# Performance work log

Hardware: AMD Instinct MI355X
Metric: run time of the kernel (lower is better)

## Reference

```python
import jax, jax.numpy as jnp
import numpy as np

V, E, H, L, F, NQ, C = 32000, 256, 8, 4, 1024, 256, 10
B, S = 8, 1024
DK = E // H


def setup_inputs() -> dict:
    key = jax.random.key(0)
    ks = jax.random.split(key, 10)
    f = lambda k, shape, s=0.02: jax.random.normal(k, shape, jnp.float32) * s
    return {
        'tokens': jax.random.randint(ks[0], (B, S), 0, V, jnp.int32),
        'emb': f(ks[1], (V, E), 1.0),
        'theta_attn': f(ks[2], (L, H, DK), 0.5),
        'Wc': f(ks[3], (L, E, E)),
        'bc': jnp.zeros((L, E), jnp.float32),
        'g1': jnp.ones((L, E), jnp.float32),
        'bn1': jnp.zeros((L, E), jnp.float32),
        'theta_ffn': f(ks[4], (L, NQ), 0.5),
        'W1': f(ks[5], (L, NQ, F)),
        'b1': jnp.zeros((L, F), jnp.float32),
        'W2': f(ks[6], (L, F, E)),
        'b2': jnp.zeros((L, E), jnp.float32),
        'g2': jnp.ones((L, E), jnp.float32),
        'bn2': jnp.zeros((L, E), jnp.float32),
        'Wcls': f(ks[7], (E, C)),
        'bcls': jnp.zeros((C,), jnp.float32),
    }


def _ln(x, g, b, eps=1e-5):
    m = x.mean(-1, keepdims=True)
    v = ((x - m) ** 2).mean(-1, keepdims=True)
    return (x - m) / jnp.sqrt(v + eps) * g + b


def _pos_encoding(seq, dim):
    pos = jnp.arange(seq, dtype=jnp.float32)[:, None]
    div = jnp.exp(jnp.arange(0, dim, 2, dtype=jnp.float32) * (-np.log(10000.0) / dim))
    pe = jnp.zeros((seq, dim), jnp.float32)
    pe = pe.at[:, 0::2].set(jnp.sin(pos * div)).at[:, 1::2].set(jnp.cos(pos * div))
    return pe


def _qattn_proj(xh, theta):
    # xh: [B,S,H,dk], theta: [H,dk]. Circuit RX(x+th) per wire, CNOT ring, <Z_i>.
    # Analytic: <Z_i> = prod_{j<=i} cos(phi_j) for i>=1; <Z_0> = prod_{j>=1} cos(phi_j)
    c = jnp.cos(xh + theta)              # [B,S,H,dk]
    cum = jnp.cumprod(c, axis=-1)        # cum[...,i] = prod_{j<=i} c_j
    head0 = jnp.prod(c[..., 1:], axis=-1, keepdims=True)
    return jnp.concatenate([head0, cum[..., 1:]], axis=-1)  # [B,S,H,dk]


def _forward(tokens, emb, theta_attn, Wc, bc, g1, bn1, theta_ffn, W1, b1, W2, b2, g2, bn2, Wcls, bcls):
    b, s = tokens.shape
    x = emb[tokens] + _pos_encoding(s, E)  # [B,S,E]
    scale = 1.0 / np.sqrt(DK)
    for l in range(L):
        # quantum multi-head projection; q = k = v (same deterministic circuit)
        xh = x.reshape(b, s, H, DK)
        p = _qattn_proj(xh, theta_attn[l]).reshape(b, s, E)
        scores = jax.nn.softmax(jnp.einsum('bqe,bke->bqk', p, p) * scale, axis=-1)
        attn = jnp.einsum('bqk,bke->bqe', scores, p) @ Wc[l] + bc[l]
        x = _ln(x + attn, g1[l], bn1[l])
        # quantum FFN: <Z_i> = cos(x_i) * cos(theta_i), NQ == E here
        q = jnp.cos(x[..., :NQ]) * jnp.cos(theta_ffn[l])
        f = jax.nn.relu(q @ W1[l] + b1[l]) @ W2[l] + b2[l]
        x = _ln(x + f, g2[l], bn2[l])
    return x.mean(axis=1) @ Wcls + bcls  # [B,C]


def reference(tokens, emb, theta_attn, Wc, bc, g1, bn1, theta_ffn, W1, b1, W2, b2, g2, bn2, Wcls, bcls):
    return _forward(tokens, emb, theta_attn, Wc, bc, g1, bn1, theta_ffn, W1, b1, W2, b2, g2, bn2, Wcls, bcls)
```

## Files before the change

kernel.cpp:

```cpp
#include <hip/hip_runtime.h>
#include <hip/hip_bf16.h>
#include <math.h>

#define BB 8
#define SS 1024
#define EE 256
#define HH 8
#define DKK 32
#define LL 4
#define FF 1024
#define NQQ 256
#define CC 10

typedef __attribute__((ext_vector_type(8))) short short8;
typedef __attribute__((ext_vector_type(4))) short s16x4;
typedef __attribute__((ext_vector_type(4))) float f32x4;

static __device__ __forceinline__ f32x4 mfma16(short8 a, short8 b, f32x4 c) {
    return __builtin_amdgcn_mfma_f32_16x16x32_bf16(a, b, c, 0, 0, 0);
}
static __device__ __forceinline__ short f2bf(float f) {
    __hip_bfloat16 h = __float2bfloat16(f);
    return *reinterpret_cast<short*>(&h);
}

#define FRAG(P, tile, KG, kg, l) ((P) + (((size_t)((tile)*(KG) + (kg)))*64 + (l))*8)

static __device__ __forceinline__ void qproj_row(
        const float* __restrict__ xrow,
        const float* __restrict__ th,
        int b, int s, int h,
        short* __restrict__ PQ, short* __restrict__ PT) {
    float v[DKK];
    float cum = __cosf(xrow[h * DKK + 0] + th[0]);
    float prod1 = 1.0f;
    #pragma unroll
    for (int j = 1; j < DKK; ++j) {
        float c = __cosf(xrow[h * DKK + j] + th[j]);
        cum *= c;
        prod1 *= c;
        v[j] = cum;
    }
    v[0] = prod1;
    short* pq = PQ + (size_t)b * SS * EE;
    int stile = s >> 4, lr = s & 15;
    #pragma unroll
    for (int lg = 0; lg < 4; ++lg) {
        short8 u;
        #pragma unroll
        for (int j = 0; j < 8; ++j) u[j] = f2bf(v[lg*8 + j]);
        *(short8*)FRAG(pq, stile*8 + h, 1, 0, lg*16 + lr) = u;
    }
    short* pt = PT + (size_t)b * SS * EE;
    int kt = s >> 5, lgs = (s >> 3) & 3, j0 = s & 7;
    #pragma unroll
    for (int j = 0; j < DKK; ++j) {
        int e = h * DKK + j;
        FRAG(pt, e >> 4, 32, kt, lgs*16 + (e & 15))[j0] = f2bf(v[j]);
    }
}

__global__ __launch_bounds__(256) void k_prep(
        const float* __restrict__ W1, const float* __restrict__ W2,
        const float* __restrict__ Wc,
        short* __restrict__ W1P, short* __restrict__ W2P, short* __restrict__ WcP,
        const int* __restrict__ tokens, const float* __restrict__ emb,
        const float* __restrict__ theta_q,
        float* __restrict__ x, short* __restrict__ PQ, short* __restrict__ PT) {
    __shared__ float shmem[16 * 268];
    const int t = threadIdx.x;
    if (blockIdx.x < 2304) {
        int bid = blockIdx.x;
        int lyr = bid / 576, rem = bid % 576;
        const float* in; short* out; int R, C, tile;
        if (rem < 256)      { in = W1 + (size_t)lyr*NQQ*FF; out = W1P + (size_t)lyr*FF*NQQ; R = NQQ; C = FF;  tile = rem; }
        else if (rem < 512) { in = W2 + (size_t)lyr*FF*EE;  out = W2P + (size_t)lyr*EE*FF;  R = FF;  C = EE;  tile = rem - 256; }
        else                { in = Wc + (size_t)lyr*EE*EE;  out = WcP + (size_t)lyr*EE*EE;  R = EE;  C = EE;  tile = rem - 512; }
        const int KG = R >> 5;
        int tiles_c = C >> 5;
        int tc = tile % tiles_c, tr = tile / tiles_c;
        float (*tl)[33] = (float(*)[33])shmem;
        int rr = t >> 5, cc = t & 31;
        #pragma unroll
        for (int i = 0; i < 4; ++i)
            tl[rr + i*8][cc] = in[(size_t)(tr*32 + rr + i*8) * C + tc*32 + cc];
        __syncthreads();
        int ro = t >> 3, co = (t & 7) * 4;
        int n = tc*32 + ro;
        int k = tr*32 + co;
        int ntile = n >> 4, lr = n & 15;
        int kg = k >> 5, lg = (k & 31) >> 3, j0 = k & 7;
        s16x4 v;
        v[0] = f2bf(tl[co + 0][ro]);
        v[1] = f2bf(tl[co + 1][ro]);
        v[2] = f2bf(tl[co + 2][ro]);
        v[3] = f2bf(tl[co + 3][ro]);
        *(s16x4*)(FRAG(out, ntile, KG, kg, lg*16 + lr) + j0) = v;
    } else {
        int blk = blockIdx.x - 2304;
        int bsw = blk & 7, local = blk >> 3;
        int tok0 = bsw * SS + local * 16;
        {
            int r = t >> 4, c0 = (t & 15) * 16;
            int bs = tok0 + r;
            int s  = bs & (SS - 1);
            int tok = tokens[bs];
            const float* er = emb + (size_t)tok * EE + c0;
            float vals[16];
            #pragma unroll
            for (int i = 0; i < 16; ++i) {
                int col = c0 + i;
                int i2 = col >> 1;
                float div = __expf(-(float)(2 * i2) * (logf(10000.0f) / (float)EE));
                float ang = (float)s * div;
                float pe = (col & 1) ? __cosf(ang) : __sinf(ang);
                vals[i] = er[i] + pe;
                shmem[r * 268 + col] = vals[i];
            }
            float* xg = x + (size_t)bs * EE + c0;
            #pragma unroll
            for (int i4 = 0; i4 < 4; ++i4)
                *(float4*)(xg + i4 * 4) = *(const float4*)&vals[i4 * 4];
        }
        __syncthreads();
        if (t < 128) {
            int sl = t >> 3, h = t & 7;
            int bs = tok0 + sl;
            qproj_row(&shmem[sl * 268], theta_q + h * DKK,
                      bs >> 10, bs & (SS - 1), h, PQ, PT);
        }
    }
}

__global__ __launch_bounds__(256) void k_attn7(const short* __restrict__ PQ,
                                               const short* __restrict__ PT,
                                               short* __restrict__ YP) {
    const int b   = blockIdx.x & 7;
    const int qt  = blockIdx.x >> 3;
    const int tid = threadIdx.x;
    const int w   = tid >> 6;
    const int l   = tid & 63;
    const int lr  = l & 15, lg = l >> 4;
    const short* pq = PQ + (size_t)b * SS * EE;
    const short* pt = PT + (size_t)b * SS * EE;

    __shared__ float accP[2][16][264];
    __shared__ float lsL[4][16];
    __shared__ short wlds[4][16 * 40];

    short8 qf[8];
    #pragma unroll
    for (int kg = 0; kg < 8; ++kg)
        qf[kg] = *(const short8*)FRAG(pq, qt*8 + kg, 1, 0, l);

    f32x4 acc[16];
    #pragma unroll
    for (int i = 0; i < 16; ++i) acc[i] = f32x4{0.f, 0.f, 0.f, 0.f};
    float ls[4] = {0.f, 0.f, 0.f, 0.f};
    const float scale = 0.17677669529663687f;
    short* wl = wlds[w];

    for (int i = 0; i < 8; ++i) {
        const int kt = w + 4 * i;
        short8 sb0[8], sb1[8];
        #pragma unroll
        for (int kg = 0; kg < 8; ++kg) {
            sb0[kg] = *(const short8*)FRAG(pq, (2*kt)*8   + kg, 1, 0, l);
            sb1[kg] = *(const short8*)FRAG(pq, (2*kt+1)*8 + kg, 1, 0, l);
        }
        f32x4 s0a = {0.f,0.f,0.f,0.f}, s0b = {0.f,0.f,0.f,0.f};
        f32x4 s1a = {0.f,0.f,0.f,0.f}, s1b = {0.f,0.f,0.f,0.f};
        __builtin_amdgcn_s_setprio(1);
        #pragma unroll
        for (int kg = 0; kg < 4; ++kg) {
            s0a = mfma16(qf[kg], sb0[kg], s0a);
            s1a = mfma16(qf[kg], sb1[kg], s1a);
        }
        #pragma unroll
        for (int kg = 4; kg < 8; ++kg) {
            s0b = mfma16(qf[kg], sb0[kg], s0b);
            s1b = mfma16(qf[kg], sb1[kg], s1b);
        }
        __builtin_amdgcn_s_setprio(0);
        short8 pvb0[8];
        #pragma unroll
        for (int nt = 0; nt < 8; ++nt)
            pvb0[nt] = *(const short8*)FRAG(pt, nt, 32, kt, l);

        #pragma unroll
        for (int r = 0; r < 4; ++r) {
            float p0 = __expf((s0a[r] + s0b[r]) * scale);
            float p1 = __expf((s1a[r] + s1b[r]) * scale);
            ls[r] += p0 + p1;
            int q = lg * 4 + r;
            wl[q * 40 + lr]      = f2bf(p0);
            wl[q * 40 + 16 + lr] = f2bf(p1);
        }
        short8 pa = *(const short8*)(wl + lr * 40 + lg * 8);
        short8 pvb1[8];
        #pragma unroll
        for (int nt = 0; nt < 8; ++nt)
            pvb1[nt] = *(const short8*)FRAG(pt, 8 + nt, 32, kt, l);
        __builtin_amdgcn_s_setprio(1);
        #pragma unroll
        for (int nt = 0; nt < 8; ++nt)
            acc[nt] = mfma16(pa, pvb0[nt], acc[nt]);
        #pragma unroll
        for (int nt = 0; nt < 8; ++nt)
            acc[8 + nt] = mfma16(pa, pvb1[nt], acc[8 + nt]);
        __builtin_amdgcn_s_setprio(0);
    }

    #pragma unroll
    for (int r = 0; r < 4; ++r) {
        ls[r] += __shfl_xor(ls[r], 1);
        ls[r] += __shfl_xor(ls[r], 2);
        ls[r] += __shfl_xor(ls[r], 4);
        ls[r] += __shfl_xor(ls[r], 8);
    }
    if (lr == 0) {
        #pragma unroll
        for (int r = 0; r < 4; ++r)
            lsL[w][lg * 4 + r] = ls[r];
    }

    if (w >= 2) {
        #pragma unroll
        for (int nt = 0; nt < 16; ++nt)
            #pragma unroll
            for (int r = 0; r < 4; ++r)
                accP[w - 2][lg * 4 + r][nt * 16 + lr] = acc[nt][r];
    }
    __syncthreads();
    if (w < 2) {
        #pragma unroll
        for (int nt = 0; nt < 16; ++nt)
            #pragma unroll
            for (int r = 0; r < 4; ++r)
                accP[w][lg * 4 + r][nt * 16 + lr] += acc[nt][r];
    }
    __syncthreads();

    const int q = tid >> 4, c = tid & 15;
    float L = lsL[0][q] + lsL[1][q] + lsL[2][q] + lsL[3][q];
    float inv = 1.0f / L;
    short ov[16];
    #pragma unroll
    for (int j = 0; j < 4; ++j) {
        float4 a  = *(const float4*)&accP[0][q][c * 16 + j * 4];
        float4 bb = *(const float4*)&accP[1][q][c * 16 + j * 4];
        ov[j*4 + 0] = f2bf((a.x + bb.x) * inv);
        ov[j*4 + 1] = f2bf((a.y + bb.y) * inv);
        ov[j*4 + 2] = f2bf((a.z + bb.z) * inv);
        ov[j*4 + 3] = f2bf((a.w + bb.w) * inv);
    }
    short* yb = YP + (size_t)b * SS * EE;
    int kgo = c >> 1, lgo = (c & 1) * 2;
    *(short8*)FRAG(yb, qt*8 + kgo, 1, 0, lgo*16 + q)     = *(const short8*)&ov[0];
    *(short8*)FRAG(yb, qt*8 + kgo, 1, 0, (lgo+1)*16 + q) = *(const short8*)&ov[8];
}

__global__ __launch_bounds__(512) void k_wcffnq(
        const short* __restrict__ YP, const short* __restrict__ WcP,
        const float* __restrict__ bc, const float* __restrict__ g1,
        const float* __restrict__ bn1,
        const float* __restrict__ tf, const short* __restrict__ W1P,
        const float* __restrict__ b1, const short* __restrict__ W2P,
        const float* __restrict__ b2, const float* __restrict__ g2,
        const float* __restrict__ bn2,
        float* __restrict__ x,
        const float* __restrict__ theta_q, short* __restrict__ PQ,
        short* __restrict__ PT, float* __restrict__ hpart, int has_next) {
    const int t = threadIdx.x, w = t >> 6, l = t & 63;
    const int lr = l & 15, lg = l >> 4;
    const int wg = w >> 2, wn = w & 3;
    const int b = blockIdx.x & 7;
    const int local = blockIdx.x >> 3;
    const int tok0 = b * SS + local * 32;
    const int qt0 = local * 2;

    __shared__ __align__(16) char smem[34304 + 16384 + 16384];
    float* outw = (float*)smem;
    char*  qls  = smem + 34304;
    char*  hls  = smem + 34304 + 16384;
    float* fout = (float*)(smem + 34304);

    const short* yb = YP + (size_t)b * SS * EE;

    {
        short8 af[8];
        #pragma unroll
        for (int kg = 0; kg < 8; ++kg)
            af[kg] = *(const short8*)FRAG(yb, (qt0 + wg)*8 + kg, 1, 0, l);
        f32x4 acc[4];
        #pragma unroll
        for (int i = 0; i < 4; ++i) acc[i] = f32x4{0.f,0.f,0.f,0.f};
        __builtin_amdgcn_s_setprio(1);
        #pragma unroll
        for (int nt = 0; nt < 4; ++nt) {
            #pragma unroll
            for (int kg = 0; kg < 8; ++kg) {
                short8 bv = *(const short8*)FRAG(WcP, wn*4 + nt, 8, kg, l);
                acc[nt] = mfma16(af[kg], bv, acc[nt]);
            }
        }
        __builtin_amdgcn_s_setprio(0);
        #pragma unroll
        for (int nt = 0; nt < 4; ++nt) {
            int e = wn * 64 + nt * 16 + lr;
            float bce = bc[e];
            #pragma unroll
            for (int r = 0; r < 4; ++r)
                outw[(wg*16 + lg*4 + r) * 268 + e] = acc[nt][r] + bce;
        }
    }
    __syncthreads();

    #pragma unroll
    for (int j = 0; j < 4; ++j) {
        int q = w * 4 + j;
        float4 v  = *(float4*)&outw[q * 268 + l * 4];
        float4 xv = *(const float4*)(x + (size_t)(tok0 + q) * EE + l * 4);
        v.x += xv.x; v.y += xv.y; v.z += xv.z; v.w += xv.w;
        float s = v.x + v.y + v.z + v.w;
        for (int off = 32; off > 0; off >>= 1) s += __shfl_xor(s, off);
        float mean = s * (1.0f / EE);
        float4 d;
        d.x = v.x - mean; d.y = v.y - mean; d.z = v.z - mean; d.w = v.w - mean;
        float s2 = d.x*d.x + d.y*d.y + d.z*d.z + d.w*d.w;
        for (int off = 32; off > 0; off >>= 1) s2 += __shfl_xor(s2, off);
        float inv = rsqrtf(s2 * (1.0f / EE) + 1e-5f);
        float4 gv  = *(const float4*)(g1  + l * 4);
        float4 bnv = *(const float4*)(bn1 + l * 4);
        float4 o;
        o.x = d.x * inv * gv.x + bnv.x;
        o.y = d.y * inv * gv.y + bnv.y;
        o.z = d.z * inv * gv.z + bnv.z;
        o.w = d.w * inv * gv.w + bnv.w;
        *(float4*)&outw[q * 268 + l * 4] = o;
        float4 tv = *(const float4*)(tf + l * 4);
        float q0 = __cosf(o.x) * __cosf(tv.x);
        float q1 = __cosf(o.y) * __cosf(tv.y);
        float q2 = __cosf(o.z) * __cosf(tv.z);
        float q3 = __cosf(o.w) * __cosf(tv.w);
        int byte = (q * 512 + l * 8) ^ ((q & 7) << 4);
        *(unsigned*)(qls + byte) =
            (unsigned)(unsigned short)f2bf(q0) | ((unsigned)(unsigned short)f2bf(q1) << 16);
        *(unsigned*)(qls + byte + 4) =
            (unsigned)(unsigned short)f2bf(q2) | ((unsigned)(unsigned short)f2bf(q3) << 16);
    }
    __syncthreads();

    f32x4 acc2[2][2];
    #pragma unroll
    for (int mt = 0; mt < 2; ++mt)
        #pragma unroll
        for (int nt = 0; nt < 2; ++nt) acc2[mt][nt] = f32x4{0.f,0.f,0.f,0.f};

    for (int fc = 0; fc < 4; ++fc) {
        f32x4 acc1[2][2];
        #pragma unroll
        for (int mt = 0; mt < 2; ++mt)
            #pragma unroll
            for (int i = 0; i < 2; ++i) acc1[mt][i] = f32x4{0.f,0.f,0.f,0.f};
        __builtin_amdgcn_s_setprio(1);
        #pragma unroll
        for (int kg = 0; kg < 8; ++kg) {
            int ca = (kg*32 + lg*8) * 2;
            short8 a0 = *(const short8*)(qls + ((lr*512      + ca) ^ ((lr & 7) << 4)));
            short8 a1 = *(const short8*)(qls + (((16+lr)*512 + ca) ^ ((lr & 7) << 4)));
            #pragma unroll
            for (int i = 0; i < 2; ++i) {
                short8 bv = *(const short8*)FRAG(W1P, fc*16 + w*2 + i, 8, kg, l);
                acc1[0][i] = mfma16(a0, bv, acc1[0][i]);
                acc1[1][i] = mfma16(a1, bv, acc1[1][i]);
            }
        }
        __builtin_amdgcn_s_setprio(0);
        #pragma unroll
        for (int mt = 0; mt < 2; ++mt) {
            #pragma unroll
            for (int i = 0; i < 2; ++i) {
                int fg   = (fc*16 + w*2 + i) * 16 + lr;
                int fcol = (w*2 + i) * 16 + lr;
                float bb = b1[fg];
                #pragma unroll
                for (int r = 0; r < 4; ++r) {
                    int tq = mt * 16 + lg * 4 + r;
                    float hv = fmaxf(acc1[mt][i][r] + bb, 0.0f);
                    int byte = (tq * 512 + fcol * 2) ^ ((tq & 7) << 4);
                    *(short*)(hls + byte) = f2bf(hv);
                }
            }
        }
        __syncthreads();
        __builtin_amdgcn_s_setprio(1);
        #pragma unroll
        for (int k8 = 0; k8 < 8; ++k8) {
            int ca = (k8*32 + lg*8) * 2;
            short8 h0 = *(const short8*)(hls + ((lr*512      + ca) ^ ((lr & 7) << 4)));
            short8 h1 = *(const short8*)(hls + (((16+lr)*512 + ca) ^ ((lr & 7) << 4)));
            #pragma unroll
            for (int nt = 0; nt < 2; ++nt) {
                short8 bv = *(const short8*)FRAG(W2P, w*2 + nt, 32, fc*8 + k8, l);
                acc2[0][nt] = mfma16(h0, bv, acc2[0][nt]);
                acc2[1][nt] = mfma16(h1, bv, acc2[1][nt]);
            }
        }
        __builtin_amdgcn_s_setprio(0);
        __syncthreads();
    }

    #pragma unroll
    for (int mt = 0; mt < 2; ++mt) {
        #pragma unroll
        for (int nt = 0; nt < 2; ++nt) {
            int e = (w*2 + nt) * 16 + lr;
            float b2e = b2[e];
            #pragma unroll
            for (int r = 0; r < 4; ++r)
                fout[(mt*16 + lg*4 + r) * 256 + e] = acc2[mt][nt][r] + b2e;
        }
    }
    __syncthreads();

    #pragma unroll
    for (int j = 0; j < 4; ++j) {
        int q = w * 4 + j;
        float4 v  = *(float4*)&fout[q * 256 + l * 4];
        float4 x1 = *(float4*)&outw[q * 268 + l * 4];
        v.x += x1.x; v.y += x1.y; v.z += x1.z; v.w += x1.w;
        float s = v.x + v.y + v.z + v.w;
        for (int off = 32; off > 0; off >>= 1) s += __shfl_xor(s, off);
        float mean = s * (1.0f / EE);
        float4 d;
        d.x = v.x - mean; d.y = v.y - mean; d.z = v.z - mean; d.w = v.w - mean;
        float s2 = d.x*d.x + d.y*d.y + d.z*d.z + d.w*d.w;
        for (int off = 32; off > 0; off >>= 1) s2 += __shfl_xor(s2, off);
        float inv = rsqrtf(s2 * (1.0f / EE) + 1e-5f);
        float4 gv  = *(const float4*)(g2  + l * 4);
        float4 bnv = *(const float4*)(bn2 + l * 4);
        float4 o;
        o.x = d.x * inv * gv.x + bnv.x;
        o.y = d.y * inv * gv.y + bnv.y;
        o.z = d.z * inv * gv.z + bnv.z;
        o.w = d.w * inv * gv.w + bnv.w;
        if (has_next)
            *(float4*)(x + (size_t)(tok0 + q) * EE + l * 4) = o;
        *(float4*)&outw[q * 268 + l * 4] = o;
    }
    __syncthreads();

    if (has_next) {
        if (t < 256) {
            int sl = t >> 3, h = t & 7;
            int bs = tok0 + sl;
            qproj_row(&outw[sl * 268], theta_q + h * DKK,
                      bs >> 10, bs & (SS - 1), h, PQ, PT);
        }
    } else {
        if (t < 256) {
            float acc = 0.0f;
            #pragma unroll 8
            for (int r = 0; r < 32; ++r)
                acc += outw[r * 268 + t];
            hpart[(size_t)(b * 32 + local) * EE + t] = acc;
        }
    }
}

__global__ __launch_bounds__(256) void k_head2(const float* __restrict__ hpart,
                                               const float* __restrict__ Wcls,
                                               const float* __restrict__ bcls,
                                               float* __restrict__ out) {
    int b = blockIdx.x;
    int t = threadIdx.x;
    __shared__ float xm[EE];
    float acc = 0.0f;
    #pragma unroll 8
    for (int j = 0; j < 32; ++j)
        acc += hpart[(size_t)(b * 32 + j) * EE + t];
    xm[t] = acc * (1.0f / (float)SS);
    __syncthreads();
    if (t < CC) {
        float a = bcls[t];
        #pragma unroll 8
        for (int e = 0; e < EE; ++e) a += xm[e] * Wcls[e * CC + t];
        out[b * CC + t] = a;
    }
}

extern "C" void kernel_launch(void* const* d_in, const int* in_sizes, int n_in,
                              void* d_out, int out_size, void* d_ws, size_t ws_size,
                              hipStream_t stream) {
    (void)in_sizes; (void)n_in; (void)out_size; (void)ws_size;
    const int*   tokens     = (const int*)d_in[0];
    const float* emb        = (const float*)d_in[1];
    const float* theta_attn = (const float*)d_in[2];
    const float* Wc         = (const float*)d_in[3];
    const float* bc         = (const float*)d_in[4];
    const float* g1         = (const float*)d_in[5];
    const float* bn1        = (const float*)d_in[6];
    const float* theta_ffn  = (const float*)d_in[7];
    const float* W1         = (const float*)d_in[8];
    const float* b1         = (const float*)d_in[9];
    const float* W2         = (const float*)d_in[10];
    const float* b2         = (const float*)d_in[11];
    const float* g2         = (const float*)d_in[12];
    const float* bn2        = (const float*)d_in[13];
    const float* Wcls       = (const float*)d_in[14];
    const float* bcls       = (const float*)d_in[15];
    float* out = (float*)d_out;

    const size_t nTok = (size_t)BB * SS * EE;
    float* x     = (float*)d_ws;
    short* PQ    = (short*)(x + nTok);
    short* PT    = PQ  + nTok;
    short* YP    = PT  + nTok;
    short* W1P   = YP  + nTok;
    short* W2P   = W1P + (size_t)LL * FF * NQQ;
    short* WcP   = W2P + (size_t)LL * EE * FF;
    float* hpart = (float*)(WcP + (size_t)LL * EE * EE);

    k_prep<<<2304 + 512, 256, 0, stream>>>(
        W1, W2, Wc, W1P, W2P, WcP, tokens, emb, theta_attn, x, PQ, PT);

    for (int l = 0; l < LL; ++l) {
        int has_next = (l + 1 < LL) ? 1 : 0;
        const float* thq = theta_attn + (size_t)(has_next ? l + 1 : 0) * HH * DKK;
        k_attn7<<<BB * 64, 256, 0, stream>>>(PQ, PT, YP);
        k_wcffnq<<<(BB * SS) / 32, 512, 0, stream>>>(
            YP, WcP + (size_t)l * EE * EE, bc + (size_t)l * EE,
            g1 + (size_t)l * EE, bn1 + (size_t)l * EE,
            theta_ffn + (size_t)l * NQQ,
            W1P + (size_t)l * FF * NQQ, b1 + (size_t)l * FF,
            W2P + (size_t)l * EE * FF, b2 + (size_t)l * EE,
            g2 + (size_t)l * EE, bn2 + (size_t)l * EE,
            x, thq, PQ, PT, hpart, has_next);
    }

    k_head2<<<BB, 256, 0, stream>>>(hpart, Wcls, bcls, out);
}
```

Measured before the change: 281.5 us.

## Double FFN kernel block to 1024 threads and drop MFMA priority hints

```diff
diff --git a/kernel.cpp b/kernel.cpp
--- a/kernel.cpp
+++ b/kernel.cpp
@@ -170,7 +170,6 @@
         }
         f32x4 s0a = {0.f,0.f,0.f,0.f}, s0b = {0.f,0.f,0.f,0.f};
         f32x4 s1a = {0.f,0.f,0.f,0.f}, s1b = {0.f,0.f,0.f,0.f};
-        __builtin_amdgcn_s_setprio(1);
         #pragma unroll
         for (int kg = 0; kg < 4; ++kg) {
             s0a = mfma16(qf[kg], sb0[kg], s0a);
@@ -181,7 +180,6 @@
             s0b = mfma16(qf[kg], sb0[kg], s0b);
             s1b = mfma16(qf[kg], sb1[kg], s1b);
         }
-        __builtin_amdgcn_s_setprio(0);
         short8 pvb0[8];
         #pragma unroll
         for (int nt = 0; nt < 8; ++nt)
@@ -201,14 +199,12 @@
         #pragma unroll
         for (int nt = 0; nt < 8; ++nt)
             pvb1[nt] = *(const short8*)FRAG(pt, 8 + nt, 32, kt, l);
-        __builtin_amdgcn_s_setprio(1);
         #pragma unroll
         for (int nt = 0; nt < 8; ++nt)
             acc[nt] = mfma16(pa, pvb0[nt], acc[nt]);
         #pragma unroll
         for (int nt = 0; nt < 8; ++nt)
             acc[8 + nt] = mfma16(pa, pvb1[nt], acc[8 + nt]);
-        __builtin_amdgcn_s_setprio(0);
     }
 
     #pragma unroll
@@ -260,7 +256,7 @@
     *(short8*)FRAG(yb, qt*8 + kgo, 1, 0, (lgo+1)*16 + q) = *(const short8*)&ov[8];
 }
 
-__global__ __launch_bounds__(512) void k_wcffnq(
+__global__ __launch_bounds__(1024) void k_wcffnq(
         const short* __restrict__ YP, const short* __restrict__ WcP,
         const float* __restrict__ bc, const float* __restrict__ g1,
         const float* __restrict__ bn1,
@@ -273,7 +269,6 @@
         short* __restrict__ PT, float* __restrict__ hpart, int has_next) {
     const int t = threadIdx.x, w = t >> 6, l = t & 63;
     const int lr = l & 15, lg = l >> 4;
-    const int wg = w >> 2, wn = w & 3;
     const int b = blockIdx.x & 7;
     const int local = blockIdx.x >> 3;
     const int tok0 = b * SS + local * 32;
@@ -288,26 +283,25 @@
     const short* yb = YP + (size_t)b * SS * EE;
 
     {
+        const int wg = w >> 3, wn8 = w & 7;
         short8 af[8];
         #pragma unroll
         for (int kg = 0; kg < 8; ++kg)
             af[kg] = *(const short8*)FRAG(yb, (qt0 + wg)*8 + kg, 1, 0, l);
-        f32x4 acc[4];
-        #pragma unroll
-        for (int i = 0; i < 4; ++i) acc[i] = f32x4{0.f,0.f,0.f,0.f};
-        __builtin_amdgcn_s_setprio(1);
-        #pragma unroll
-        for (int nt = 0; nt < 4; ++nt) {
+        f32x4 acc[2];
+        acc[0] = f32x4{0.f,0.f,0.f,0.f};
+        acc[1] = f32x4{0.f,0.f,0.f,0.f};
+        #pragma unroll
+        for (int nt = 0; nt < 2; ++nt) {
             #pragma unroll
             for (int kg = 0; kg < 8; ++kg) {
-                short8 bv = *(const short8*)FRAG(WcP, wn*4 + nt, 8, kg, l);
+                short8 bv = *(const short8*)FRAG(WcP, wn8*2 + nt, 8, kg, l);
                 acc[nt] = mfma16(af[kg], bv, acc[nt]);
             }
         }
-        __builtin_amdgcn_s_setprio(0);
-        #pragma unroll
-        for (int nt = 0; nt < 4; ++nt) {
-            int e = wn * 64 + nt * 16 + lr;
+        #pragma unroll
+        for (int nt = 0; nt < 2; ++nt) {
+            int e = wn8 * 32 + nt * 16 + lr;
             float bce = bc[e];
             #pragma unroll
             for (int r = 0; r < 4; ++r)
@@ -317,8 +311,8 @@
     __syncthreads();
 
     #pragma unroll
-    for (int j = 0; j < 4; ++j) {
-        int q = w * 4 + j;
+    for (int j = 0; j < 2; ++j) {
+        int q = w * 2 + j;
         float4 v  = *(float4*)&outw[q * 268 + l * 4];
         float4 xv = *(const float4*)(x + (size_t)(tok0 + q) * EE + l * 4);
         v.x += xv.x; v.y += xv.y; v.z += xv.z; v.w += xv.w;
@@ -351,82 +345,64 @@
     }
     __syncthreads();
 
-    f32x4 acc2[2][2];
-    #pragma unroll
-    for (int mt = 0; mt < 2; ++mt)
-        #pragma unroll
-        for (int nt = 0; nt < 2; ++nt) acc2[mt][nt] = f32x4{0.f,0.f,0.f,0.f};
+    f32x4 acc2[2];
+    acc2[0] = f32x4{0.f,0.f,0.f,0.f};
+    acc2[1] = f32x4{0.f,0.f,0.f,0.f};
 
     for (int fc = 0; fc < 4; ++fc) {
-        f32x4 acc1[2][2];
-        #pragma unroll
-        for (int mt = 0; mt < 2; ++mt)
-            #pragma unroll
-            for (int i = 0; i < 2; ++i) acc1[mt][i] = f32x4{0.f,0.f,0.f,0.f};
-        __builtin_amdgcn_s_setprio(1);
+        f32x4 acc1[2];
+        acc1[0] = f32x4{0.f,0.f,0.f,0.f};
+        acc1[1] = f32x4{0.f,0.f,0.f,0.f};
         #pragma unroll
         for (int kg = 0; kg < 8; ++kg) {
             int ca = (kg*32 + lg*8) * 2;
             short8 a0 = *(const short8*)(qls + ((lr*512      + ca) ^ ((lr & 7) << 4)));
             short8 a1 = *(const short8*)(qls + (((16+lr)*512 + ca) ^ ((lr & 7) << 4)));
-            #pragma unroll
-            for (int i = 0; i < 2; ++i) {
-                short8 bv = *(const short8*)FRAG(W1P, fc*16 + w*2 + i, 8, kg, l);
-                acc1[0][i] = mfma16(a0, bv, acc1[0][i]);
-                acc1[1][i] = mfma16(a1, bv, acc1[1][i]);
-            }
-        }
-        __builtin_amdgcn_s_setprio(0);
-        #pragma unroll
-        for (int mt = 0; mt < 2; ++mt) {
-            #pragma unroll
-            for (int i = 0; i < 2; ++i) {
-                int fg   = (fc*16 + w*2 + i) * 16 + lr;
-                int fcol = (w*2 + i) * 16 + lr;
-                float bb = b1[fg];
+            short8 bv = *(const short8*)FRAG(W1P, fc*16 + w, 8, kg, l);
+            acc1[0] = mfma16(a0, bv, acc1[0]);
+            acc1[1] = mfma16(a1, bv, acc1[1]);
+        }
+        {
+            int fcol = w * 16 + lr;
+            float bb = b1[fc * 256 + fcol];
+            #pragma unroll
+            for (int mt = 0; mt < 2; ++mt) {
                 #pragma unroll
                 for (int r = 0; r < 4; ++r) {
                     int tq = mt * 16 + lg * 4 + r;
-                    float hv = fmaxf(acc1[mt][i][r] + bb, 0.0f);
+                    float hv = fmaxf(acc1[mt][r] + bb, 0.0f);
                     int byte = (tq * 512 + fcol * 2) ^ ((tq & 7) << 4);
                     *(short*)(hls + byte) = f2bf(hv);
                 }
             }
         }
         __syncthreads();
-        __builtin_amdgcn_s_setprio(1);
         #pragma unroll
         for (int k8 = 0; k8 < 8; ++k8) {
             int ca = (k8*32 + lg*8) * 2;
             short8 h0 = *(const short8*)(hls + ((lr*512      + ca) ^ ((lr & 7) << 4)));
             short8 h1 = *(const short8*)(hls + (((16+lr)*512 + ca) ^ ((lr & 7) << 4)));
-            #pragma unroll
-            for (int nt = 0; nt < 2; ++nt) {
-                short8 bv = *(const short8*)FRAG(W2P, w*2 + nt, 32, fc*8 + k8, l);
-                acc2[0][nt] = mfma16(h0, bv, acc2[0][nt]);
-                acc2[1][nt] = mfma16(h1, bv, acc2[1][nt]);
-            }
-        }
-        __builtin_amdgcn_s_setprio(0);
+            short8 bv = *(const short8*)FRAG(W2P, w, 32, fc*8 + k8, l);
+            acc2[0] = mfma16(h0, bv, acc2[0]);
+            acc2[1] = mfma16(h1, bv, acc2[1]);
+        }
         __syncthreads();
     }
 
-    #pragma unroll
-    for (int mt = 0; mt < 2; ++mt) {
-        #pragma unroll
-        for (int nt = 0; nt < 2; ++nt) {
-            int e = (w*2 + nt) * 16 + lr;
-            float b2e = b2[e];
+    {
+        int e = w * 16 + lr;
+        float b2e = b2[e];
+        #pragma unroll
+        for (int mt = 0; mt < 2; ++mt)
             #pragma unroll
             for (int r = 0; r < 4; ++r)
-                fout[(mt*16 + lg*4 + r) * 256 + e] = acc2[mt][nt][r] + b2e;
-        }
-    }
-    __syncthreads();
-
-    #pragma unroll
-    for (int j = 0; j < 4; ++j) {
-        int q = w * 4 + j;
+                fout[(mt*16 + lg*4 + r) * 256 + e] = acc2[mt][r] + b2e;
+    }
+    __syncthreads();
+
+    #pragma unroll
+    for (int j = 0; j < 2; ++j) {
+        int q = w * 2 + j;
         float4 v  = *(float4*)&fout[q * 256 + l * 4];
         float4 x1 = *(float4*)&outw[q * 268 + l * 4];
         v.x += x1.x; v.y += x1.y; v.z += x1.z; v.w += x1.w;
@@ -529,7 +505,7 @@
         int has_next = (l + 1 < LL) ? 1 : 0;
         const float* thq = theta_attn + (size_t)(has_next ? l + 1 : 0) * HH * DKK;
         k_attn7<<<BB * 64, 256, 0, stream>>>(PQ, PT, YP);
-        k_wcffnq<<<(BB * SS) / 32, 512, 0, stream>>>(
+        k_wcffnq<<<(BB * SS) / 32, 1024, 0, stream>>>(
             YP, WcP + (size_t)l * EE * EE, bc + (size_t)l * EE,
             g1 + (size_t)l * EE, bn1 + (size_t)l * EE,
             theta_ffn + (size_t)l * NQQ,
```

After: 247.7 us, median of 2. -12.0%, faster.
